# Kernel tuning notes

Measured on AMD Instinct MI355X. Metric: run time of the kernel, lower is better.

## Reference

```python
import jax, jax.numpy as jnp
import numpy as np

EPS_F = 1e-12
M, N = 64, 4096  # feature dim m, num nodes n


def setup_inputs() -> dict:
    key = jax.random.key(0)
    k1, k2, k3, k4 = jax.random.split(key, 4)
    # X: (m, n) node features transposed, as in the repo (features.t())
    X = jax.random.normal(k1, (M, N), dtype=jnp.float32)
    # F: (m, m) parameter, xavier_uniform init
    bound = float(np.sqrt(6.0 / (M + M)))
    F = jax.random.uniform(k2, (M, M), minval=-bound, maxval=bound, dtype=jnp.float32)
    # Q_S: (n, n) orthogonal eigenvector matrix of the (symmetric, normalized) adjacency
    A = jax.random.normal(k3, (N, N), dtype=jnp.float32)
    Q_S, _ = jnp.linalg.qr(A)
    Q_S = Q_S.astype(jnp.float32)
    # Lambda_S: (n, 1) eigenvalues of normalized adjacency, inside (-1, 1)
    Lambda_S = jnp.sort(
        jax.random.uniform(k4, (N, 1), minval=-0.95, maxval=0.95, dtype=jnp.float32), axis=0
    )
    gamma = jnp.asarray(0.8, dtype=jnp.float32)
    return {"X": X, "F": F, "Q_S": Q_S, "Lambda_S": Lambda_S, "gamma": gamma}


def reference(X, F, Q_S, Lambda_S, gamma):
    # g(F) = F^T F / (||F^T F||_F + eps)  -- Frobenius-normalized Gram matrix
    FF = F.T @ F                                   # (m, m)
    G_F = FF / (jnp.linalg.norm(FF) + EPS_F)       # (m, m), symmetric PSD, ||.||_F ~ 1
    # spectral decomposition of g(F)
    Lambda_F, Q_F = jnp.linalg.eigh(G_F)           # (m,), (m, m)
    # closed-form equilibrium of Z = gamma * g(F) Z S^T + X in the joint eigenbasis
    D = 1.0 / (1.0 - gamma * Lambda_F[:, None] * Lambda_S.reshape(1, -1))  # (m, n)
    Z = Q_F @ (D * (Q_F.T @ X @ Q_S)) @ Q_S.T      # (m, n)
    return Z
```

## Files before the change

kernel.cpp:

```cpp
#include <hip/hip_runtime.h>
#include <math.h>


typedef short short8 __attribute__((ext_vector_type(8)));
typedef float floatx16 __attribute__((ext_vector_type(16)));

#define KSPLIT 16
#define KCHUNK 256
constexpr int Mdim = 64;
constexpr int Ndim = 4096;
constexpr int TILE = Mdim * Ndim;

__device__ inline ushort f2bf(float f) {
    uint u = __float_as_uint(f);
    u += 0x7fff + ((u >> 16) & 1);
    return (ushort)(u >> 16);
}
__device__ inline float bf2f(ushort h) { return __uint_as_float(((uint)h) << 16); }

__device__ inline floatx16 mfma_bf16(short8 a, short8 b, floatx16 c) {
    return __builtin_amdgcn_mfma_f32_32x32x16_bf16(a, b, c, 0, 0, 0);
}

struct SharedGemm { ushort Ah[4096], Al[4096], Bh[4096]; };

__device__ inline void barrier_nodrain() {
    asm volatile("s_waitcnt lgkmcnt(0)" ::: "memory");
    __builtin_amdgcn_s_barrier();
    __builtin_amdgcn_sched_barrier(0);
}

__device__ void prep_body(SharedGemm& sg, const float* __restrict__ F, float* __restrict__ Gout) {
    const int t = threadIdx.x;
    const int l = t & 63, w = t >> 6;
    const int tm = w & 1, tn = w >> 1;
    const int am = tm * 32 + (l & 31);
    const int bn = tn * 32 + (l & 31);
    const int lk = l >> 5;
    float* red = (float*)sg.Bh;

    {
        const int r = t >> 2, c0 = (t & 3) * 16;
#pragma unroll
        for (int q = 0; q < 4; ++q) {
            float4 v = *(const float4*)&F[r * 64 + c0 + 4 * q];
            float fa[4] = {v.x, v.y, v.z, v.w};
#pragma unroll
            for (int i = 0; i < 4; ++i) {
                int c = c0 + 4 * q + i;
                ushort h = f2bf(fa[i]);
                int idx = c * 64 + (((r >> 3) ^ (c & 7)) * 8) + (r & 7);
                sg.Ah[idx] = h;
                sg.Al[idx] = f2bf(fa[i] - bf2f(h));
            }
        }
    }
    __syncthreads();
    floatx16 acc;
    for (int i = 0; i < 16; ++i) acc[i] = 0.f;
    for (int s16 = 0; s16 < 4; ++s16) {
        int gk = 2 * s16 + lk;
        int ai = am * 64 + ((gk ^ (am & 7)) * 8);
        int bi = bn * 64 + ((gk ^ (bn & 7)) * 8);
        short8 ah = *(const short8*)&sg.Ah[ai];
        short8 al = *(const short8*)&sg.Al[ai];
        short8 bh = *(const short8*)&sg.Ah[bi];
        short8 bl = *(const short8*)&sg.Al[bi];
        acc = mfma_bf16(ah, bh, acc);
        acc = mfma_bf16(al, bh, acc);
        acc = mfma_bf16(ah, bl, acc);
    }
    float ss = 0.f;
    for (int r = 0; r < 16; ++r) ss += acc[r] * acc[r];
    red[t] = ss;
    __syncthreads();
    for (int off = 128; off > 0; off >>= 1) {
        if (t < off) red[t] += red[t + off];
        __syncthreads();
    }
    const float inv = 1.0f / (sqrtf(red[0]) + 1e-12f);
    for (int r = 0; r < 16; ++r) {
        int row = (r & 3) + 8 * (r >> 2) + 4 * lk + tm * 32;
        int col = tn * 32 + (l & 31);
        float v = acc[r] * inv;
        Gout[row * 64 + col] = v;
        ushort h = f2bf(v);
        int idx = row * 64 + (((col >> 3) ^ (row & 7)) * 8 + (col & 7));
        sg.Ah[idx] = h;
        sg.Al[idx] = f2bf(v - bf2f(h));
    }
    for (int j = 1; j < 5; ++j) {
        __syncthreads();
        floatx16 a2;
        for (int i = 0; i < 16; ++i) a2[i] = 0.f;
        for (int s16 = 0; s16 < 4; ++s16) {
            int gk = 2 * s16 + lk;
            int ai = am * 64 + ((gk ^ (am & 7)) * 8);
            int bi = bn * 64 + ((gk ^ (bn & 7)) * 8);
            short8 ah = *(const short8*)&sg.Ah[ai];
            short8 al = *(const short8*)&sg.Al[ai];
            short8 bh = *(const short8*)&sg.Ah[bi];
            short8 bl = *(const short8*)&sg.Al[bi];
            a2 = mfma_bf16(ah, bh, a2);
            a2 = mfma_bf16(al, bh, a2);
            a2 = mfma_bf16(ah, bl, a2);
        }
        __syncthreads();
        for (int r = 0; r < 16; ++r) {
            int row = (r & 3) + 8 * (r >> 2) + 4 * lk + tm * 32;
            int col = tn * 32 + (l & 31);
            float v = a2[r];
            Gout[j * 4096 + row * 64 + col] = v;
            ushort h = f2bf(v);
            int idx = row * 64 + (((col >> 3) ^ (row & 7)) * 8 + (col & 7));
            sg.Ah[idx] = h;
            sg.Al[idx] = f2bf(v - bf2f(h));
        }
    }
}

template <bool TB>
__device__ inline void load_b(float4 (&dst)[4], const float* __restrict__ Bm,
                              int n0, int kk, int sr, int sj, int nq, int kr2) {
    if constexpr (TB) {
#pragma unroll
        for (int s = 0; s < 4; ++s)
            dst[s] = *(const float4*)&Bm[(size_t)(n0 + sr) * 4096 + kk + 4 * sj + 16 * s];
    } else {
#pragma unroll
        for (int s = 0; s < 2; ++s) {
            dst[2 * s + 0] = *(const float4*)&Bm[(size_t)(kk + kr2 + 32 * s) * 4096 + n0 + 4 * nq];
            dst[2 * s + 1] = *(const float4*)&Bm[(size_t)(kk + kr2 + 1 + 32 * s) * 4096 + n0 + 4 * nq];
        }
    }
}

template <bool TB, bool DOPREP>
__global__ __launch_bounds__(256, 4) void gemm_kernel(const float* __restrict__ A,
                                                      const float* __restrict__ Bm,
                                                      float* __restrict__ C,
                                                      const float* __restrict__ F,
                                                      float* __restrict__ Gp) {
    __shared__ SharedGemm sh;
    const int bid = blockIdx.x;
    if (DOPREP) {
        if (bid == 0) { prep_body(sh, F, Gp); return; }
    }
    const int b = DOPREP ? bid - 1 : bid;
    const int n0 = (b & 63) * 64;
    const int ks = b >> 6;
    const int kb = ks * KCHUNK;
    const int t = threadIdx.x;
    const int l = t & 63, w = t >> 6;
    const int tm = w & 1, tn = w >> 1;
    const int am = tm * 32 + (l & 31);
    const int bn = tn * 32 + (l & 31);
    const int lk = l >> 5;
    const int sr = t >> 2, sj = t & 3;
    const int nq = t & 15, kr2 = 2 * (t >> 4);

    floatx16 acc;
    for (int i = 0; i < 16; ++i) acc[i] = 0.f;

    float4 bbuf[4][4];
    load_b<TB>(bbuf[0], Bm, n0, kb, sr, sj, nq, kr2);
    load_b<TB>(bbuf[1], Bm, n0, kb + 64, sr, sj, nq, kr2);

#pragma unroll
    for (int step = 0; step < KCHUNK / 64; ++step) {
        const int k0 = kb + step * 64;
        float4 av[4];
#pragma unroll
        for (int s = 0; s < 4; ++s)
            av[s] = *(const float4*)&A[sr * 4096 + k0 + 4 * sj + 16 * s];
        if (step + 2 < KCHUNK / 64)
            load_b<TB>(bbuf[step + 2], Bm, n0, k0 + 128, sr, sj, nq, kr2);
        barrier_nodrain();
        if (TB) {
#pragma unroll
            for (int s = 0; s < 4; ++s) {
                int off = 4 * sj + 16 * s;
                int idx = sr * 64 + (((off >> 3) ^ (sr & 7)) * 8 + (off & 7));
                float fb[4] = {bbuf[step][s].x, bbuf[step][s].y, bbuf[step][s].z, bbuf[step][s].w};
                ushort4 h4;
                ushort* hp = (ushort*)&h4;
#pragma unroll
                for (int i = 0; i < 4; ++i) hp[i] = f2bf(fb[i]);
                *(ushort4*)&sh.Bh[idx] = h4;
            }
        } else {
#pragma unroll
            for (int s = 0; s < 2; ++s) {
                int k = kr2 + 32 * s;
                float fa[4] = {bbuf[step][2 * s].x, bbuf[step][2 * s].y, bbuf[step][2 * s].z, bbuf[step][2 * s].w};
                float fb[4] = {bbuf[step][2 * s + 1].x, bbuf[step][2 * s + 1].y, bbuf[step][2 * s + 1].z, bbuf[step][2 * s + 1].w};
#pragma unroll
                for (int i = 0; i < 4; ++i) {
                    int n = 4 * nq + i;
                    int idx = n * 64 + (((k >> 3) ^ (n & 7)) * 8 + (k & 7));
                    ushort2 hp2;
                    hp2.x = f2bf(fa[i]);
                    hp2.y = f2bf(fb[i]);
                    *(ushort2*)&sh.Bh[idx] = hp2;
                }
            }
        }
#pragma unroll
        for (int s = 0; s < 4; ++s) {
            int off = 4 * sj + 16 * s;
            int idx = sr * 64 + (((off >> 3) ^ (sr & 7)) * 8 + (off & 7));
            float fa[4] = {av[s].x, av[s].y, av[s].z, av[s].w};
            ushort4 h4, l4;
            ushort* hp = (ushort*)&h4; ushort* lp = (ushort*)&l4;
#pragma unroll
            for (int i = 0; i < 4; ++i) {
                ushort h = f2bf(fa[i]);
                hp[i] = h; lp[i] = f2bf(fa[i] - bf2f(h));
            }
            *(ushort4*)&sh.Ah[idx] = h4;
            *(ushort4*)&sh.Al[idx] = l4;
        }
        barrier_nodrain();
#pragma unroll
        for (int s16 = 0; s16 < 4; ++s16) {
            int gk = 2 * s16 + lk;
            int ai = am * 64 + ((gk ^ (am & 7)) * 8);
            int bi = bn * 64 + ((gk ^ (bn & 7)) * 8);
            short8 ah = *(const short8*)&sh.Ah[ai];
            short8 al = *(const short8*)&sh.Al[ai];
            short8 bh = *(const short8*)&sh.Bh[bi];
            acc = mfma_bf16(ah, bh, acc);
            acc = mfma_bf16(al, bh, acc);
        }
    }
    float* Cp = C + (size_t)ks * TILE;
    const int colg = n0 + tn * 32 + (l & 31);
#pragma unroll
    for (int r = 0; r < 16; ++r) {
        int row = (r & 3) + 8 * (r >> 2) + 4 * lk + tm * 32;
        Cp[row * 4096 + colg] = acc[r];
    }
}

__global__ __launch_bounds__(256) void reduce_kernel(const float* __restrict__ P,
                                                     float* __restrict__ out) {
    const int i = blockIdx.x * 256 + threadIdx.x;
    float4 a = {0.f, 0.f, 0.f, 0.f};
#pragma unroll
    for (int s = 0; s < KSPLIT; ++s) {
        const float4 v = *(const float4*)&P[(size_t)s * TILE + 4 * i];
        a.x += v.x; a.y += v.y; a.z += v.z; a.w += v.w;
    }
    *(float4*)&out[4 * i] = a;
}

__global__ __launch_bounds__(256) void solve_kernel(const float* __restrict__ W,
                                                    const float* __restrict__ Gp,
                                                    const float* __restrict__ lam,
                                                    const float* __restrict__ gammap,
                                                    float* __restrict__ Y) {
    __shared__ float Gs[64][68];
    __shared__ float T[64][17];
    const int t = threadIdx.x;
    const int c0 = blockIdx.x * 16;
    for (int e = t; e < 1024; e += 256)
        T[e >> 4][e & 15] = W[(e >> 4) * 4096 + c0 + (e & 15)];
    const int tx = t & 15;
    const int r4 = (t >> 4) * 4;
    const float a = gammap[0] * lam[c0 + tx];
    float s = a;
    for (int j = 0; j < 5; ++j) {
        __syncthreads();
        for (int e = t; e < 4096; e += 256) Gs[e >> 6][e & 63] = Gp[j * 4096 + e];
        __syncthreads();
        float u0 = 0.f, u1 = 0.f, u2 = 0.f, u3 = 0.f;
#pragma unroll 8
        for (int k = 0; k < 64; ++k) {
            const float tv = T[k][tx];
            const float4 g = *(const float4*)&Gs[k][r4];
            u0 += g.x * tv; u1 += g.y * tv; u2 += g.z * tv; u3 += g.w * tv;
        }
        __syncthreads();
        T[r4 + 0][tx] += s * u0;
        T[r4 + 1][tx] += s * u1;
        T[r4 + 2][tx] += s * u2;
        T[r4 + 3][tx] += s * u3;
        s = s * s;
    }
    __syncthreads();
    for (int e = t; e < 1024; e += 256)
        Y[(e >> 4) * 4096 + c0 + (e & 15)] = T[e >> 4][e & 15];
}

extern "C" void kernel_launch(void* const* d_in, const int* in_sizes, int n_in,
                              void* d_out, int out_size, void* d_ws, size_t ws_size,
                              hipStream_t stream) {
    const float* X     = (const float*)d_in[0];
    const float* F     = (const float*)d_in[1];
    const float* Qs    = (const float*)d_in[2];
    const float* lam   = (const float*)d_in[3];
    const float* gamma = (const float*)d_in[4];
    float* Z = (float*)d_out;

    float* P  = (float*)d_ws;
    float* W  = P + (size_t)KSPLIT * TILE;
    float* Y  = W + TILE;
    float* Gp = Y + TILE;

    gemm_kernel<false, true><<<64 * KSPLIT + 1, 256, 0, stream>>>(X, Qs, P, F, Gp);
    reduce_kernel<<<256, 256, 0, stream>>>(P, W);
    solve_kernel<<<Ndim / 16, 256, 0, stream>>>(W, Gp, lam, gamma, Y);
    gemm_kernel<true, false><<<64 * KSPLIT, 256, 0, stream>>>(Y, Qs, P, nullptr, nullptr);
    reduce_kernel<<<256, 256, 0, stream>>>(P, Z);
}
```

Baseline: 155.4 us.

## Fuse all stages into one persistent kernel with software grid barriers

Replaces five separate launches (gemm+prep, reduce, solve, gemm, reduce) with a single 1024-block kernel that uses atomic-counter grid barriers between phases. The solve phase folds in the split-K reduction and writes Y pre-split into bf16 hi/lo planes in an MFMA-fragment layout, so the second GEMM loads A fragments straight from global memory and double-buffers its B tile in LDS. The goal is to remove launch gaps and intermediate global round-trips. In exchange it depends on all 1024 blocks being co-resident (4 per CU), adds a memset launch, and gives the solve phase only 4 columns per block.

```diff
diff --git a/kernel.cpp b/kernel.cpp
--- a/kernel.cpp
+++ b/kernel.cpp
@@ -10,6 +10,7 @@
 constexpr int Mdim = 64;
 constexpr int Ndim = 4096;
 constexpr int TILE = Mdim * Ndim;
+constexpr int NBLK = 1024;
 
 __device__ inline ushort f2bf(float f) {
     uint u = __float_as_uint(f);
@@ -22,7 +23,12 @@
     return __builtin_amdgcn_mfma_f32_32x32x16_bf16(a, b, c, 0, 0, 0);
 }
 
-struct SharedGemm { ushort Ah[4096], Al[4096], Bh[4096]; };
+union SharedU {
+    struct { ushort Ah[4096], Al[4096], Bh[4096]; } g1;
+    struct { ushort Bh[2][4096]; } g3;
+    struct { ushort planes[2][4096]; float red[256]; } p;
+    struct { float Gs[64][66]; float T[64][5]; float Tp[4][64][4]; } s;
+};
 
 __device__ inline void barrier_nodrain() {
     asm volatile("s_waitcnt lgkmcnt(0)" ::: "memory");
@@ -30,14 +36,34 @@
     __builtin_amdgcn_sched_barrier(0);
 }
 
-__device__ void prep_body(SharedGemm& sg, const float* __restrict__ F, float* __restrict__ Gout) {
+__device__ inline void grid_barrier(uint* bar, int idx) {
+    __syncthreads();
+    if (threadIdx.x == 0) {
+        __threadfence();
+        uint* cnt  = bar + idx * 64;
+        uint* flag = bar + idx * 64 + 32;
+        uint old = __hip_atomic_fetch_add(cnt, 1u, __ATOMIC_ACQ_REL, __HIP_MEMORY_SCOPE_AGENT);
+        if (old == (uint)NBLK - 1) {
+            __hip_atomic_store(flag, 1u, __ATOMIC_RELEASE, __HIP_MEMORY_SCOPE_AGENT);
+        } else {
+            while (!__hip_atomic_load(flag, __ATOMIC_RELAXED, __HIP_MEMORY_SCOPE_AGENT))
+                __builtin_amdgcn_s_sleep(1);
+        }
+        __threadfence();
+    }
+    __syncthreads();
+}
+
+__device__ void prep_body(SharedU& sh, const float* __restrict__ F, float* __restrict__ Gout) {
     const int t = threadIdx.x;
     const int l = t & 63, w = t >> 6;
     const int tm = w & 1, tn = w >> 1;
     const int am = tm * 32 + (l & 31);
     const int bn = tn * 32 + (l & 31);
     const int lk = l >> 5;
-    float* red = (float*)sg.Bh;
+    ushort* Ph = sh.p.planes[0];
+    ushort* Pl = sh.p.planes[1];
+    float* red = sh.p.red;
 
     {
         const int r = t >> 2, c0 = (t & 3) * 16;
@@ -50,22 +76,22 @@
                 int c = c0 + 4 * q + i;
                 ushort h = f2bf(fa[i]);
                 int idx = c * 64 + (((r >> 3) ^ (c & 7)) * 8) + (r & 7);
-                sg.Ah[idx] = h;
-                sg.Al[idx] = f2bf(fa[i] - bf2f(h));
+                Ph[idx] = h;
+                Pl[idx] = f2bf(fa[i] - bf2f(h));
             }
         }
     }
-    __syncthreads();
+    barrier_nodrain();
     floatx16 acc;
     for (int i = 0; i < 16; ++i) acc[i] = 0.f;
     for (int s16 = 0; s16 < 4; ++s16) {
         int gk = 2 * s16 + lk;
         int ai = am * 64 + ((gk ^ (am & 7)) * 8);
         int bi = bn * 64 + ((gk ^ (bn & 7)) * 8);
-        short8 ah = *(const short8*)&sg.Ah[ai];
-        short8 al = *(const short8*)&sg.Al[ai];
-        short8 bh = *(const short8*)&sg.Ah[bi];
-        short8 bl = *(const short8*)&sg.Al[bi];
+        short8 ah = *(const short8*)&Ph[ai];
+        short8 al = *(const short8*)&Pl[ai];
+        short8 bh = *(const short8*)&Ph[bi];
+        short8 bl = *(const short8*)&Pl[bi];
         acc = mfma_bf16(ah, bh, acc);
         acc = mfma_bf16(al, bh, acc);
         acc = mfma_bf16(ah, bl, acc);
@@ -73,10 +99,10 @@
     float ss = 0.f;
     for (int r = 0; r < 16; ++r) ss += acc[r] * acc[r];
     red[t] = ss;
-    __syncthreads();
+    barrier_nodrain();
     for (int off = 128; off > 0; off >>= 1) {
         if (t < off) red[t] += red[t + off];
-        __syncthreads();
+        barrier_nodrain();
     }
     const float inv = 1.0f / (sqrtf(red[0]) + 1e-12f);
     for (int r = 0; r < 16; ++r) {
@@ -86,26 +112,26 @@
         Gout[row * 64 + col] = v;
         ushort h = f2bf(v);
         int idx = row * 64 + (((col >> 3) ^ (row & 7)) * 8 + (col & 7));
-        sg.Ah[idx] = h;
-        sg.Al[idx] = f2bf(v - bf2f(h));
+        Ph[idx] = h;
+        Pl[idx] = f2bf(v - bf2f(h));
     }
     for (int j = 1; j < 5; ++j) {
-        __syncthreads();
+        barrier_nodrain();
         floatx16 a2;
         for (int i = 0; i < 16; ++i) a2[i] = 0.f;
         for (int s16 = 0; s16 < 4; ++s16) {
             int gk = 2 * s16 + lk;
             int ai = am * 64 + ((gk ^ (am & 7)) * 8);
             int bi = bn * 64 + ((gk ^ (bn & 7)) * 8);
-            short8 ah = *(const short8*)&sg.Ah[ai];
-            short8 al = *(const short8*)&sg.Al[ai];
-            short8 bh = *(const short8*)&sg.Ah[bi];
-            short8 bl = *(const short8*)&sg.Al[bi];
+            short8 ah = *(const short8*)&Ph[ai];
+            short8 al = *(const short8*)&Pl[ai];
+            short8 bh = *(const short8*)&Ph[bi];
+            short8 bl = *(const short8*)&Pl[bi];
             a2 = mfma_bf16(ah, bh, a2);
             a2 = mfma_bf16(al, bh, a2);
             a2 = mfma_bf16(ah, bl, a2);
         }
-        __syncthreads();
+        barrier_nodrain();
         for (int r = 0; r < 16; ++r) {
             int row = (r & 3) + 8 * (r >> 2) + 4 * lk + tm * 32;
             int col = tn * 32 + (l & 31);
@@ -113,8 +139,8 @@
             Gout[j * 4096 + row * 64 + col] = v;
             ushort h = f2bf(v);
             int idx = row * 64 + (((col >> 3) ^ (row & 7)) * 8 + (col & 7));
-            sg.Ah[idx] = h;
-            sg.Al[idx] = f2bf(v - bf2f(h));
+            Ph[idx] = h;
+            Pl[idx] = f2bf(v - bf2f(h));
         }
     }
 }
@@ -135,22 +161,11 @@
     }
 }
 
-template <bool TB, bool DOPREP>
-__global__ __launch_bounds__(256, 4) void gemm_kernel(const float* __restrict__ A,
-                                                      const float* __restrict__ Bm,
-                                                      float* __restrict__ C,
-                                                      const float* __restrict__ F,
-                                                      float* __restrict__ Gp) {
-    __shared__ SharedGemm sh;
-    const int bid = blockIdx.x;
-    if (DOPREP) {
-        if (bid == 0) { prep_body(sh, F, Gp); return; }
-    }
-    const int b = DOPREP ? bid - 1 : bid;
-    const int n0 = (b & 63) * 64;
-    const int ks = b >> 6;
+__device__ void gemm_lds(SharedU& sh, const float* __restrict__ A, const float* __restrict__ Bm,
+                         float* __restrict__ C, int tile, int t) {
+    const int n0 = (tile & 63) * 64;
+    const int ks = tile >> 6;
     const int kb = ks * KCHUNK;
-    const int t = threadIdx.x;
     const int l = t & 63, w = t >> 6;
     const int tm = w & 1, tn = w >> 1;
     const int am = tm * 32 + (l & 31);
@@ -163,8 +178,8 @@
     for (int i = 0; i < 16; ++i) acc[i] = 0.f;
 
     float4 bbuf[4][4];
-    load_b<TB>(bbuf[0], Bm, n0, kb, sr, sj, nq, kr2);
-    load_b<TB>(bbuf[1], Bm, n0, kb + 64, sr, sj, nq, kr2);
+    load_b<false>(bbuf[0], Bm, n0, kb, sr, sj, nq, kr2);
+    load_b<false>(bbuf[1], Bm, n0, kb + 64, sr, sj, nq, kr2);
 
 #pragma unroll
     for (int step = 0; step < KCHUNK / 64; ++step) {
@@ -174,35 +189,21 @@
         for (int s = 0; s < 4; ++s)
             av[s] = *(const float4*)&A[sr * 4096 + k0 + 4 * sj + 16 * s];
         if (step + 2 < KCHUNK / 64)
-            load_b<TB>(bbuf[step + 2], Bm, n0, k0 + 128, sr, sj, nq, kr2);
-        barrier_nodrain();
-        if (TB) {
-#pragma unroll
-            for (int s = 0; s < 4; ++s) {
-                int off = 4 * sj + 16 * s;
-                int idx = sr * 64 + (((off >> 3) ^ (sr & 7)) * 8 + (off & 7));
-                float fb[4] = {bbuf[step][s].x, bbuf[step][s].y, bbuf[step][s].z, bbuf[step][s].w};
-                ushort4 h4;
-                ushort* hp = (ushort*)&h4;
-#pragma unroll
-                for (int i = 0; i < 4; ++i) hp[i] = f2bf(fb[i]);
-                *(ushort4*)&sh.Bh[idx] = h4;
-            }
-        } else {
-#pragma unroll
-            for (int s = 0; s < 2; ++s) {
-                int k = kr2 + 32 * s;
-                float fa[4] = {bbuf[step][2 * s].x, bbuf[step][2 * s].y, bbuf[step][2 * s].z, bbuf[step][2 * s].w};
-                float fb[4] = {bbuf[step][2 * s + 1].x, bbuf[step][2 * s + 1].y, bbuf[step][2 * s + 1].z, bbuf[step][2 * s + 1].w};
-#pragma unroll
-                for (int i = 0; i < 4; ++i) {
-                    int n = 4 * nq + i;
-                    int idx = n * 64 + (((k >> 3) ^ (n & 7)) * 8 + (k & 7));
-                    ushort2 hp2;
-                    hp2.x = f2bf(fa[i]);
-                    hp2.y = f2bf(fb[i]);
-                    *(ushort2*)&sh.Bh[idx] = hp2;
-                }
+            load_b<false>(bbuf[step + 2], Bm, n0, k0 + 128, sr, sj, nq, kr2);
+        barrier_nodrain();
+#pragma unroll
+        for (int s = 0; s < 2; ++s) {
+            int k = kr2 + 32 * s;
+            float fa[4] = {bbuf[step][2 * s].x, bbuf[step][2 * s].y, bbuf[step][2 * s].z, bbuf[step][2 * s].w};
+            float fb[4] = {bbuf[step][2 * s + 1].x, bbuf[step][2 * s + 1].y, bbuf[step][2 * s + 1].z, bbuf[step][2 * s + 1].w};
+#pragma unroll
+            for (int i = 0; i < 4; ++i) {
+                int n = 4 * nq + i;
+                int idx = n * 64 + (((k >> 3) ^ (n & 7)) * 8 + (k & 7));
+                ushort2 hp2;
+                hp2.x = f2bf(fa[i]);
+                hp2.y = f2bf(fb[i]);
+                *(ushort2*)&sh.g1.Bh[idx] = hp2;
             }
         }
 #pragma unroll
@@ -217,8 +218,8 @@
                 ushort h = f2bf(fa[i]);
                 hp[i] = h; lp[i] = f2bf(fa[i] - bf2f(h));
             }
-            *(ushort4*)&sh.Ah[idx] = h4;
-            *(ushort4*)&sh.Al[idx] = l4;
+            *(ushort4*)&sh.g1.Ah[idx] = h4;
+            *(ushort4*)&sh.g1.Al[idx] = l4;
         }
         barrier_nodrain();
 #pragma unroll
@@ -226,9 +227,9 @@
             int gk = 2 * s16 + lk;
             int ai = am * 64 + ((gk ^ (am & 7)) * 8);
             int bi = bn * 64 + ((gk ^ (bn & 7)) * 8);
-            short8 ah = *(const short8*)&sh.Ah[ai];
-            short8 al = *(const short8*)&sh.Al[ai];
-            short8 bh = *(const short8*)&sh.Bh[bi];
+            short8 ah = *(const short8*)&sh.g1.Ah[ai];
+            short8 al = *(const short8*)&sh.g1.Al[ai];
+            short8 bh = *(const short8*)&sh.g1.Bh[bi];
             acc = mfma_bf16(ah, bh, acc);
             acc = mfma_bf16(al, bh, acc);
         }
@@ -242,54 +243,144 @@
     }
 }
 
-__global__ __launch_bounds__(256) void reduce_kernel(const float* __restrict__ P,
-                                                     float* __restrict__ out) {
-    const int i = blockIdx.x * 256 + threadIdx.x;
-    float4 a = {0.f, 0.f, 0.f, 0.f};
-#pragma unroll
-    for (int s = 0; s < KSPLIT; ++s) {
-        const float4 v = *(const float4*)&P[(size_t)s * TILE + 4 * i];
-        a.x += v.x; a.y += v.y; a.z += v.z; a.w += v.w;
-    }
-    *(float4*)&out[4 * i] = a;
-}
-
-__global__ __launch_bounds__(256) void solve_kernel(const float* __restrict__ W,
-                                                    const float* __restrict__ Gp,
-                                                    const float* __restrict__ lam,
-                                                    const float* __restrict__ gammap,
-                                                    float* __restrict__ Y) {
-    __shared__ float Gs[64][68];
-    __shared__ float T[64][17];
-    const int t = threadIdx.x;
-    const int c0 = blockIdx.x * 16;
-    for (int e = t; e < 1024; e += 256)
-        T[e >> 4][e & 15] = W[(e >> 4) * 4096 + c0 + (e & 15)];
-    const int tx = t & 15;
-    const int r4 = (t >> 4) * 4;
-    const float a = gammap[0] * lam[c0 + tx];
-    float s = a;
+__device__ void gemm_direct(SharedU& sh, const ushort* __restrict__ Yh, const ushort* __restrict__ Yl,
+                            const float* __restrict__ Bm, float* __restrict__ C, int tile, int t) {
+    const int n0 = (tile & 63) * 64;
+    const int ks = tile >> 6;
+    const int kb = ks * KCHUNK;
+    const int l = t & 63, w = t >> 6;
+    const int tm = w & 1, tn = w >> 1;
+    const int am = tm * 32 + (l & 31);
+    const int bn = tn * 32 + (l & 31);
+    const int lk = l >> 5;
+    const int sr = t >> 2, sj = t & 3;
+
+    floatx16 acc;
+    for (int i = 0; i < 16; ++i) acc[i] = 0.f;
+
+    float4 bbuf[3][4];
+    load_b<true>(bbuf[0], Bm, n0, kb, sr, sj, 0, 0);
+    load_b<true>(bbuf[1], Bm, n0, kb + 64, sr, sj, 0, 0);
+
+#pragma unroll
+    for (int step = 0; step < KCHUNK / 64; ++step) {
+        const int k0 = kb + step * 64;
+        const int par = step & 1;
+        const int slot = step % 3;
+        if (step + 2 < KCHUNK / 64)
+            load_b<true>(bbuf[(step + 2) % 3], Bm, n0, k0 + 128, sr, sj, 0, 0);
+        short8 afh[4], afl[4];
+#pragma unroll
+        for (int s16 = 0; s16 < 4; ++s16) {
+            int gk = (k0 >> 3) + 2 * s16 + lk;
+            afh[s16] = *(const short8*)&Yh[gk * 512 + am * 8];
+            afl[s16] = *(const short8*)&Yl[gk * 512 + am * 8];
+        }
+#pragma unroll
+        for (int s = 0; s < 4; ++s) {
+            int off = 4 * sj + 16 * s;
+            int idx = sr * 64 + (((off >> 3) ^ (sr & 7)) * 8 + (off & 7));
+            float fb[4] = {bbuf[slot][s].x, bbuf[slot][s].y, bbuf[slot][s].z, bbuf[slot][s].w};
+            ushort4 h4;
+            ushort* hp = (ushort*)&h4;
+#pragma unroll
+            for (int i = 0; i < 4; ++i) hp[i] = f2bf(fb[i]);
+            *(ushort4*)&sh.g3.Bh[par][idx] = h4;
+        }
+        barrier_nodrain();
+#pragma unroll
+        for (int s16 = 0; s16 < 4; ++s16) {
+            int gk = 2 * s16 + lk;
+            int bi = bn * 64 + ((gk ^ (bn & 7)) * 8);
+            short8 bh = *(const short8*)&sh.g3.Bh[par][bi];
+            acc = mfma_bf16(afh[s16], bh, acc);
+            acc = mfma_bf16(afl[s16], bh, acc);
+        }
+    }
+    float* Cp = C + (size_t)ks * TILE;
+    const int colg = n0 + tn * 32 + (l & 31);
+#pragma unroll
+    for (int r = 0; r < 16; ++r) {
+        int row = (r & 3) + 8 * (r >> 2) + 4 * lk + tm * 32;
+        Cp[row * 4096 + colg] = acc[r];
+    }
+}
+
+__device__ void solve_body(SharedU& sh, const float* __restrict__ P1, const float* __restrict__ Gp,
+                           const float* __restrict__ lam, const float* __restrict__ gam,
+                           ushort* __restrict__ Yh, ushort* __restrict__ Yl, int bid, int t) {
+    const int c0 = bid * 4;
+    {
+        const int r = t & 63, sg = t >> 6;
+        float4 a = {0.f, 0.f, 0.f, 0.f};
+#pragma unroll
+        for (int s = 0; s < 4; ++s) {
+            const float4 v = *(const float4*)&P1[(size_t)(sg * 4 + s) * TILE + (size_t)r * 4096 + c0];
+            a.x += v.x; a.y += v.y; a.z += v.z; a.w += v.w;
+        }
+        *(float4*)&sh.s.Tp[sg][r][0] = a;
+    }
+    barrier_nodrain();
+    if (t < 64) {
+        const int r = t;
+        float4 a0 = *(const float4*)&sh.s.Tp[0][r][0];
+        float4 a1 = *(const float4*)&sh.s.Tp[1][r][0];
+        float4 a2 = *(const float4*)&sh.s.Tp[2][r][0];
+        float4 a3 = *(const float4*)&sh.s.Tp[3][r][0];
+        sh.s.T[r][0] = a0.x + a1.x + a2.x + a3.x;
+        sh.s.T[r][1] = a0.y + a1.y + a2.y + a3.y;
+        sh.s.T[r][2] = a0.z + a1.z + a2.z + a3.z;
+        sh.s.T[r][3] = a0.w + a1.w + a2.w + a3.w;
+    }
+    barrier_nodrain();
+    const int r = t >> 2, c = t & 3;
+    float ap = gam[0] * lam[c0 + c];
     for (int j = 0; j < 5; ++j) {
-        __syncthreads();
-        for (int e = t; e < 4096; e += 256) Gs[e >> 6][e & 63] = Gp[j * 4096 + e];
-        __syncthreads();
-        float u0 = 0.f, u1 = 0.f, u2 = 0.f, u3 = 0.f;
+        for (int e = t; e < 4096; e += 256) sh.s.Gs[e >> 6][e & 63] = Gp[j * 4096 + e];
+        barrier_nodrain();
+        float u = 0.f;
 #pragma unroll 8
-        for (int k = 0; k < 64; ++k) {
-            const float tv = T[k][tx];
-            const float4 g = *(const float4*)&Gs[k][r4];
-            u0 += g.x * tv; u1 += g.y * tv; u2 += g.z * tv; u3 += g.w * tv;
-        }
-        __syncthreads();
-        T[r4 + 0][tx] += s * u0;
-        T[r4 + 1][tx] += s * u1;
-        T[r4 + 2][tx] += s * u2;
-        T[r4 + 3][tx] += s * u3;
-        s = s * s;
-    }
-    __syncthreads();
-    for (int e = t; e < 1024; e += 256)
-        Y[(e >> 4) * 4096 + c0 + (e & 15)] = T[e >> 4][e & 15];
+        for (int k = 0; k < 64; ++k) u += sh.s.Gs[r][k] * sh.s.T[k][c];
+        barrier_nodrain();
+        sh.s.T[r][c] += ap * u;
+        ap = ap * ap;
+    }
+    const float v = sh.s.T[r][c];
+    const ushort h = f2bf(v);
+    const int col = c0 + c;
+    const int idx = (col >> 3) * 512 + r * 8 + (col & 7);
+    Yh[idx] = h;
+    Yl[idx] = f2bf(v - bf2f(h));
+}
+
+__global__ __launch_bounds__(256, 4) void fused_kernel(
+    const float* __restrict__ X, const float* __restrict__ F,
+    const float* __restrict__ Qs, const float* __restrict__ lam,
+    const float* __restrict__ gam, float* __restrict__ Z,
+    float* __restrict__ P1, float* __restrict__ P2, float* __restrict__ Gp,
+    ushort* __restrict__ Yh, ushort* __restrict__ Yl, uint* bar) {
+    __shared__ SharedU sh;
+    const int b = blockIdx.x, t = threadIdx.x;
+
+    if (b == 0) {
+        prep_body(sh, F, Gp);
+        gemm_lds(sh, X, Qs, P1, 0, t);
+    } else {
+        gemm_lds(sh, X, Qs, P1, b, t);
+    }
+    grid_barrier(bar, 0);
+
+    solve_body(sh, P1, Gp, lam, gam, Yh, Yl, b, t);
+    grid_barrier(bar, 1);
+
+    gemm_direct(sh, Yh, Yl, Qs, P2, b, t);
+    grid_barrier(bar, 2);
+
+    const int gi = b * 256 + t;
+    float a = 0.f;
+#pragma unroll
+    for (int s = 0; s < KSPLIT; ++s) a += P2[(size_t)s * TILE + gi];
+    Z[gi] = a;
 }
 
 extern "C" void kernel_launch(void* const* d_in, const int* in_sizes, int n_in,
@@ -302,14 +393,14 @@
     const float* gamma = (const float*)d_in[4];
     float* Z = (float*)d_out;
 
-    float* P  = (float*)d_ws;
-    float* W  = P + (size_t)KSPLIT * TILE;
-    float* Y  = W + TILE;
-    float* Gp = Y + TILE;
-
-    gemm_kernel<false, true><<<64 * KSPLIT + 1, 256, 0, stream>>>(X, Qs, P, F, Gp);
-    reduce_kernel<<<256, 256, 0, stream>>>(P, W);
-    solve_kernel<<<Ndim / 16, 256, 0, stream>>>(W, Gp, lam, gamma, Y);
-    gemm_kernel<true, false><<<64 * KSPLIT, 256, 0, stream>>>(Y, Qs, P, nullptr, nullptr);
-    reduce_kernel<<<256, 256, 0, stream>>>(P, Z);
-}
+    float* P1 = (float*)d_ws;
+    float* P2 = P1 + (size_t)KSPLIT * TILE;
+    float* Gp = P2 + (size_t)KSPLIT * TILE;
+    ushort* Yh = (ushort*)(Gp + 5 * 4096);
+    ushort* Yl = Yh + TILE;
+    uint* bar  = (uint*)(Yl + TILE);
+
+    hipMemsetAsync(bar, 0, 2048, stream);
+    fused_kernel<<<NBLK, 256, 0, stream>>>(X, F, Qs, lam, gamma, Z,
+                                           P1, P2, Gp, Yh, Yl, bar);
+}
```

Result: slower. 409.1 us (+163.2%).

## Fuse first split-K reduction into solve, pre-split Y to bf16, double K-split

Applied to the files above, without the earlier changes.

Doubles the K-split (32 chunks of 128) so more blocks are in flight for both Q_S GEMMs. The first partial-sum reduction is folded into the solve kernel, which removes one launch and one round trip of W through global memory. The solve kernel now writes Y as pre-split hi/lo bf16 planes in an MFMA-friendly layout, so the second GEMM reads A fragments straight from global memory and keeps a double-buffered LDS tile only for B. The trade-off is twice as much partial-sum traffic, and the prep block's __syncthreads calls are replaced with lighter barriers.

```diff
diff --git a/kernel.cpp b/kernel.cpp
--- a/kernel.cpp
+++ b/kernel.cpp
@@ -5,8 +5,8 @@
 typedef short short8 __attribute__((ext_vector_type(8)));
 typedef float floatx16 __attribute__((ext_vector_type(16)));
 
-#define KSPLIT 16
-#define KCHUNK 256
+#define KSPLIT 32
+#define KCHUNK 128
 constexpr int Mdim = 64;
 constexpr int Ndim = 4096;
 constexpr int TILE = Mdim * Ndim;
@@ -22,7 +22,10 @@
     return __builtin_amdgcn_mfma_f32_32x32x16_bf16(a, b, c, 0, 0, 0);
 }
 
-struct SharedGemm { ushort Ah[4096], Al[4096], Bh[4096]; };
+union SharedG1 {
+    struct { ushort Ah[4096], Al[4096], Bh[4096]; } g;
+    struct { ushort planes[2][4096]; float red[256]; } p;
+};
 
 __device__ inline void barrier_nodrain() {
     asm volatile("s_waitcnt lgkmcnt(0)" ::: "memory");
@@ -30,14 +33,16 @@
     __builtin_amdgcn_sched_barrier(0);
 }
 
-__device__ void prep_body(SharedGemm& sg, const float* __restrict__ F, float* __restrict__ Gout) {
+__device__ void prep_body(SharedG1& sh, const float* __restrict__ F, float* __restrict__ Gout) {
     const int t = threadIdx.x;
     const int l = t & 63, w = t >> 6;
     const int tm = w & 1, tn = w >> 1;
     const int am = tm * 32 + (l & 31);
     const int bn = tn * 32 + (l & 31);
     const int lk = l >> 5;
-    float* red = (float*)sg.Bh;
+    ushort* Ph = sh.p.planes[0];
+    ushort* Pl = sh.p.planes[1];
+    float* red = sh.p.red;
 
     {
         const int r = t >> 2, c0 = (t & 3) * 16;
@@ -50,22 +55,22 @@
                 int c = c0 + 4 * q + i;
                 ushort h = f2bf(fa[i]);
                 int idx = c * 64 + (((r >> 3) ^ (c & 7)) * 8) + (r & 7);
-                sg.Ah[idx] = h;
-                sg.Al[idx] = f2bf(fa[i] - bf2f(h));
+                Ph[idx] = h;
+                Pl[idx] = f2bf(fa[i] - bf2f(h));
             }
         }
     }
-    __syncthreads();
+    barrier_nodrain();
     floatx16 acc;
     for (int i = 0; i < 16; ++i) acc[i] = 0.f;
     for (int s16 = 0; s16 < 4; ++s16) {
         int gk = 2 * s16 + lk;
         int ai = am * 64 + ((gk ^ (am & 7)) * 8);
         int bi = bn * 64 + ((gk ^ (bn & 7)) * 8);
-        short8 ah = *(const short8*)&sg.Ah[ai];
-        short8 al = *(const short8*)&sg.Al[ai];
-        short8 bh = *(const short8*)&sg.Ah[bi];
-        short8 bl = *(const short8*)&sg.Al[bi];
+        short8 ah = *(const short8*)&Ph[ai];
+        short8 al = *(const short8*)&Pl[ai];
+        short8 bh = *(const short8*)&Ph[bi];
+        short8 bl = *(const short8*)&Pl[bi];
         acc = mfma_bf16(ah, bh, acc);
         acc = mfma_bf16(al, bh, acc);
         acc = mfma_bf16(ah, bl, acc);
@@ -73,10 +78,10 @@
     float ss = 0.f;
     for (int r = 0; r < 16; ++r) ss += acc[r] * acc[r];
     red[t] = ss;
-    __syncthreads();
+    barrier_nodrain();
     for (int off = 128; off > 0; off >>= 1) {
         if (t < off) red[t] += red[t + off];
-        __syncthreads();
+        barrier_nodrain();
     }
     const float inv = 1.0f / (sqrtf(red[0]) + 1e-12f);
     for (int r = 0; r < 16; ++r) {
@@ -86,26 +91,26 @@
         Gout[row * 64 + col] = v;
         ushort h = f2bf(v);
         int idx = row * 64 + (((col >> 3) ^ (row & 7)) * 8 + (col & 7));
-        sg.Ah[idx] = h;
-        sg.Al[idx] = f2bf(v - bf2f(h));
+        Ph[idx] = h;
+        Pl[idx] = f2bf(v - bf2f(h));
     }
     for (int j = 1; j < 5; ++j) {
-        __syncthreads();
+        barrier_nodrain();
         floatx16 a2;
         for (int i = 0; i < 16; ++i) a2[i] = 0.f;
         for (int s16 = 0; s16 < 4; ++s16) {
             int gk = 2 * s16 + lk;
             int ai = am * 64 + ((gk ^ (am & 7)) * 8);
             int bi = bn * 64 + ((gk ^ (bn & 7)) * 8);
-            short8 ah = *(const short8*)&sg.Ah[ai];
-            short8 al = *(const short8*)&sg.Al[ai];
-            short8 bh = *(const short8*)&sg.Ah[bi];
-            short8 bl = *(const short8*)&sg.Al[bi];
+            short8 ah = *(const short8*)&Ph[ai];
+            short8 al = *(const short8*)&Pl[ai];
+            short8 bh = *(const short8*)&Ph[bi];
+            short8 bl = *(const short8*)&Pl[bi];
             a2 = mfma_bf16(ah, bh, a2);
             a2 = mfma_bf16(al, bh, a2);
             a2 = mfma_bf16(ah, bl, a2);
         }
-        __syncthreads();
+        barrier_nodrain();
         for (int r = 0; r < 16; ++r) {
             int row = (r & 3) + 8 * (r >> 2) + 4 * lk + tm * 32;
             int col = tn * 32 + (l & 31);
@@ -113,8 +118,8 @@
             Gout[j * 4096 + row * 64 + col] = v;
             ushort h = f2bf(v);
             int idx = row * 64 + (((col >> 3) ^ (row & 7)) * 8 + (col & 7));
-            sg.Ah[idx] = h;
-            sg.Al[idx] = f2bf(v - bf2f(h));
+            Ph[idx] = h;
+            Pl[idx] = f2bf(v - bf2f(h));
         }
     }
 }
@@ -135,18 +140,15 @@
     }
 }
 
-template <bool TB, bool DOPREP>
-__global__ __launch_bounds__(256, 4) void gemm_kernel(const float* __restrict__ A,
-                                                      const float* __restrict__ Bm,
-                                                      float* __restrict__ C,
-                                                      const float* __restrict__ F,
-                                                      float* __restrict__ Gp) {
-    __shared__ SharedGemm sh;
+__global__ __launch_bounds__(256, 4) void gemm1_kernel(const float* __restrict__ A,
+                                                       const float* __restrict__ Bm,
+                                                       float* __restrict__ C,
+                                                       const float* __restrict__ F,
+                                                       float* __restrict__ Gp) {
+    __shared__ SharedG1 sh;
     const int bid = blockIdx.x;
-    if (DOPREP) {
-        if (bid == 0) { prep_body(sh, F, Gp); return; }
-    }
-    const int b = DOPREP ? bid - 1 : bid;
+    if (bid == 0) { prep_body(sh, F, Gp); return; }
+    const int b = bid - 1;
     const int n0 = (b & 63) * 64;
     const int ks = b >> 6;
     const int kb = ks * KCHUNK;
@@ -162,9 +164,9 @@
     floatx16 acc;
     for (int i = 0; i < 16; ++i) acc[i] = 0.f;
 
-    float4 bbuf[4][4];
-    load_b<TB>(bbuf[0], Bm, n0, kb, sr, sj, nq, kr2);
-    load_b<TB>(bbuf[1], Bm, n0, kb + 64, sr, sj, nq, kr2);
+    float4 bbuf[2][4];
+    load_b<false>(bbuf[0], Bm, n0, kb, sr, sj, nq, kr2);
+    load_b<false>(bbuf[1], Bm, n0, kb + 64, sr, sj, nq, kr2);
 
 #pragma unroll
     for (int step = 0; step < KCHUNK / 64; ++step) {
@@ -173,36 +175,20 @@
 #pragma unroll
         for (int s = 0; s < 4; ++s)
             av[s] = *(const float4*)&A[sr * 4096 + k0 + 4 * sj + 16 * s];
-        if (step + 2 < KCHUNK / 64)
-            load_b<TB>(bbuf[step + 2], Bm, n0, k0 + 128, sr, sj, nq, kr2);
-        barrier_nodrain();
-        if (TB) {
-#pragma unroll
-            for (int s = 0; s < 4; ++s) {
-                int off = 4 * sj + 16 * s;
-                int idx = sr * 64 + (((off >> 3) ^ (sr & 7)) * 8 + (off & 7));
-                float fb[4] = {bbuf[step][s].x, bbuf[step][s].y, bbuf[step][s].z, bbuf[step][s].w};
-                ushort4 h4;
-                ushort* hp = (ushort*)&h4;
-#pragma unroll
-                for (int i = 0; i < 4; ++i) hp[i] = f2bf(fb[i]);
-                *(ushort4*)&sh.Bh[idx] = h4;
-            }
-        } else {
-#pragma unroll
-            for (int s = 0; s < 2; ++s) {
-                int k = kr2 + 32 * s;
-                float fa[4] = {bbuf[step][2 * s].x, bbuf[step][2 * s].y, bbuf[step][2 * s].z, bbuf[step][2 * s].w};
-                float fb[4] = {bbuf[step][2 * s + 1].x, bbuf[step][2 * s + 1].y, bbuf[step][2 * s + 1].z, bbuf[step][2 * s + 1].w};
-#pragma unroll
-                for (int i = 0; i < 4; ++i) {
-                    int n = 4 * nq + i;
-                    int idx = n * 64 + (((k >> 3) ^ (n & 7)) * 8 + (k & 7));
-                    ushort2 hp2;
-                    hp2.x = f2bf(fa[i]);
-                    hp2.y = f2bf(fb[i]);
-                    *(ushort2*)&sh.Bh[idx] = hp2;
-                }
+        barrier_nodrain();
+#pragma unroll
+        for (int s = 0; s < 2; ++s) {
+            int k = kr2 + 32 * s;
+            float fa[4] = {bbuf[step][2 * s].x, bbuf[step][2 * s].y, bbuf[step][2 * s].z, bbuf[step][2 * s].w};
+            float fb[4] = {bbuf[step][2 * s + 1].x, bbuf[step][2 * s + 1].y, bbuf[step][2 * s + 1].z, bbuf[step][2 * s + 1].w};
+#pragma unroll
+            for (int i = 0; i < 4; ++i) {
+                int n = 4 * nq + i;
+                int idx = n * 64 + (((k >> 3) ^ (n & 7)) * 8 + (k & 7));
+                ushort2 hp2;
+                hp2.x = f2bf(fa[i]);
+                hp2.y = f2bf(fb[i]);
+                *(ushort2*)&sh.g.Bh[idx] = hp2;
             }
         }
 #pragma unroll
@@ -217,8 +203,8 @@
                 ushort h = f2bf(fa[i]);
                 hp[i] = h; lp[i] = f2bf(fa[i] - bf2f(h));
             }
-            *(ushort4*)&sh.Ah[idx] = h4;
-            *(ushort4*)&sh.Al[idx] = l4;
+            *(ushort4*)&sh.g.Ah[idx] = h4;
+            *(ushort4*)&sh.g.Al[idx] = l4;
         }
         barrier_nodrain();
 #pragma unroll
@@ -226,9 +212,9 @@
             int gk = 2 * s16 + lk;
             int ai = am * 64 + ((gk ^ (am & 7)) * 8);
             int bi = bn * 64 + ((gk ^ (bn & 7)) * 8);
-            short8 ah = *(const short8*)&sh.Ah[ai];
-            short8 al = *(const short8*)&sh.Al[ai];
-            short8 bh = *(const short8*)&sh.Bh[bi];
+            short8 ah = *(const short8*)&sh.g.Ah[ai];
+            short8 al = *(const short8*)&sh.g.Al[ai];
+            short8 bh = *(const short8*)&sh.g.Bh[bi];
             acc = mfma_bf16(ah, bh, acc);
             acc = mfma_bf16(al, bh, acc);
         }
@@ -242,33 +228,32 @@
     }
 }
 
-__global__ __launch_bounds__(256) void reduce_kernel(const float* __restrict__ P,
-                                                     float* __restrict__ out) {
-    const int i = blockIdx.x * 256 + threadIdx.x;
-    float4 a = {0.f, 0.f, 0.f, 0.f};
-#pragma unroll
-    for (int s = 0; s < KSPLIT; ++s) {
-        const float4 v = *(const float4*)&P[(size_t)s * TILE + 4 * i];
-        a.x += v.x; a.y += v.y; a.z += v.z; a.w += v.w;
-    }
-    *(float4*)&out[4 * i] = a;
-}
-
-__global__ __launch_bounds__(256) void solve_kernel(const float* __restrict__ W,
+__global__ __launch_bounds__(256) void solve_kernel(const float* __restrict__ P1,
                                                     const float* __restrict__ Gp,
                                                     const float* __restrict__ lam,
                                                     const float* __restrict__ gammap,
-                                                    float* __restrict__ Y) {
+                                                    ushort* __restrict__ Yh,
+                                                    ushort* __restrict__ Yl) {
     __shared__ float Gs[64][68];
     __shared__ float T[64][17];
     const int t = threadIdx.x;
     const int c0 = blockIdx.x * 16;
-    for (int e = t; e < 1024; e += 256)
-        T[e >> 4][e & 15] = W[(e >> 4) * 4096 + c0 + (e & 15)];
+    {
+        const int r = t >> 2, q = t & 3;
+        float4 a = {0.f, 0.f, 0.f, 0.f};
+        for (int s = 0; s < KSPLIT; ++s) {
+            const float4 v = *(const float4*)&P1[(size_t)s * TILE + (size_t)r * 4096 + c0 + 4 * q];
+            a.x += v.x; a.y += v.y; a.z += v.z; a.w += v.w;
+        }
+        T[r][4 * q + 0] = a.x;
+        T[r][4 * q + 1] = a.y;
+        T[r][4 * q + 2] = a.z;
+        T[r][4 * q + 3] = a.w;
+    }
     const int tx = t & 15;
     const int r4 = (t >> 4) * 4;
-    const float a = gammap[0] * lam[c0 + tx];
-    float s = a;
+    const float a0 = gammap[0] * lam[c0 + tx];
+    float s = a0;
     for (int j = 0; j < 5; ++j) {
         __syncthreads();
         for (int e = t; e < 4096; e += 256) Gs[e >> 6][e & 63] = Gp[j * 4096 + e];
@@ -288,8 +273,91 @@
         s = s * s;
     }
     __syncthreads();
-    for (int e = t; e < 1024; e += 256)
-        Y[(e >> 4) * 4096 + c0 + (e & 15)] = T[e >> 4][e & 15];
+    for (int e = t; e < 1024; e += 256) {
+        const int r = e >> 4, cc = e & 15, col = c0 + cc;
+        const float v = T[r][cc];
+        const ushort h = f2bf(v);
+        const int idx = (col >> 3) * 512 + r * 8 + (col & 7);
+        Yh[idx] = h;
+        Yl[idx] = f2bf(v - bf2f(h));
+    }
+}
+
+__global__ __launch_bounds__(256, 4) void gemm2_kernel(const ushort* __restrict__ Yh,
+                                                       const ushort* __restrict__ Yl,
+                                                       const float* __restrict__ Bm,
+                                                       float* __restrict__ C) {
+    __shared__ ushort Bhs[2][4096];
+    const int b = blockIdx.x;
+    const int n0 = (b & 63) * 64;
+    const int ks = b >> 6;
+    const int kb = ks * KCHUNK;
+    const int t = threadIdx.x;
+    const int l = t & 63, w = t >> 6;
+    const int tm = w & 1, tn = w >> 1;
+    const int am = tm * 32 + (l & 31);
+    const int bn = tn * 32 + (l & 31);
+    const int lk = l >> 5;
+    const int sr = t >> 2, sj = t & 3;
+
+    floatx16 acc;
+    for (int i = 0; i < 16; ++i) acc[i] = 0.f;
+
+    float4 bbuf[2][4];
+    load_b<true>(bbuf[0], Bm, n0, kb, sr, sj, 0, 0);
+    load_b<true>(bbuf[1], Bm, n0, kb + 64, sr, sj, 0, 0);
+
+#pragma unroll
+    for (int step = 0; step < KCHUNK / 64; ++step) {
+        const int k0 = kb + step * 64;
+        const int par = step & 1;
+        short8 afh[4], afl[4];
+#pragma unroll
+        for (int s16 = 0; s16 < 4; ++s16) {
+            int gk = (k0 >> 3) + 2 * s16 + lk;
+            afh[s16] = *(const short8*)&Yh[gk * 512 + am * 8];
+            afl[s16] = *(const short8*)&Yl[gk * 512 + am * 8];
+        }
+#pragma unroll
+        for (int s = 0; s < 4; ++s) {
+            int off = 4 * sj + 16 * s;
+            int idx = sr * 64 + (((off >> 3) ^ (sr & 7)) * 8 + (off & 7));
+            float fb[4] = {bbuf[step][s].x, bbuf[step][s].y, bbuf[step][s].z, bbuf[step][s].w};
+            ushort4 h4;
+            ushort* hp = (ushort*)&h4;
+#pragma unroll
+            for (int i = 0; i < 4; ++i) hp[i] = f2bf(fb[i]);
+            *(ushort4*)&Bhs[par][idx] = h4;
+        }
+        barrier_nodrain();
+#pragma unroll
+        for (int s16 = 0; s16 < 4; ++s16) {
+            int gk = 2 * s16 + lk;
+            int bi = bn * 64 + ((gk ^ (bn & 7)) * 8);
+            short8 bh = *(const short8*)&Bhs[par][bi];
+            acc = mfma_bf16(afh[s16], bh, acc);
+            acc = mfma_bf16(afl[s16], bh, acc);
+        }
+    }
+    float* Cp = C + (size_t)ks * TILE;
+    const int colg = n0 + tn * 32 + (l & 31);
+#pragma unroll
+    for (int r = 0; r < 16; ++r) {
+        int row = (r & 3) + 8 * (r >> 2) + 4 * lk + tm * 32;
+        Cp[row * 4096 + colg] = acc[r];
+    }
+}
+
+__global__ __launch_bounds__(256) void reduce_kernel(const float* __restrict__ P,
+                                                     float* __restrict__ out) {
+    const int i = blockIdx.x * 256 + threadIdx.x;
+    float4 a = {0.f, 0.f, 0.f, 0.f};
+#pragma unroll
+    for (int s = 0; s < KSPLIT; ++s) {
+        const float4 v = *(const float4*)&P[(size_t)s * TILE + 4 * i];
+        a.x += v.x; a.y += v.y; a.z += v.z; a.w += v.w;
+    }
+    *(float4*)&out[4 * i] = a;
 }
 
 extern "C" void kernel_launch(void* const* d_in, const int* in_sizes, int n_in,
@@ -302,14 +370,14 @@
     const float* gamma = (const float*)d_in[4];
     float* Z = (float*)d_out;
 
-    float* P  = (float*)d_ws;
-    float* W  = P + (size_t)KSPLIT * TILE;
-    float* Y  = W + TILE;
-    float* Gp = Y + TILE;
-
-    gemm_kernel<false, true><<<64 * KSPLIT + 1, 256, 0, stream>>>(X, Qs, P, F, Gp);
-    reduce_kernel<<<256, 256, 0, stream>>>(P, W);
-    solve_kernel<<<Ndim / 16, 256, 0, stream>>>(W, Gp, lam, gamma, Y);
-    gemm_kernel<true, false><<<64 * KSPLIT, 256, 0, stream>>>(Y, Qs, P, nullptr, nullptr);
-    reduce_kernel<<<256, 256, 0, stream>>>(P, Z);
-}
+    float* P1 = (float*)d_ws;
+    float* P2 = P1 + (size_t)KSPLIT * TILE;
+    float* Gp = P2 + (size_t)KSPLIT * TILE;
+    ushort* Yh = (ushort*)(Gp + 5 * 4096);
+    ushort* Yl = Yh + TILE;
+
+    gemm1_kernel<<<64 * KSPLIT + 1, 256, 0, stream>>>(X, Qs, P1, F, Gp);
+    solve_kernel<<<Ndim / 16, 256, 0, stream>>>(P1, Gp, lam, gamma, Yh, Yl);
+    gemm2_kernel<<<64 * KSPLIT, 256, 0, stream>>>(Yh, Yl, Qs, P2);
+    reduce_kernel<<<256, 256, 0, stream>>>(P2, Z);
+}
```

After: 160.5 us. +3.3%, slower.
